# Optimization experiments

Measured on AMD Instinct MI355X. Metric: run time of the kernel, lower is better.

The kernel has to match this reference:

```python
import jax, jax.numpy as jnp
import numpy as np

B, N, D, H, F = 16, 257, 1024, 16, 4096
HD = D // H
EPS = 1e-5
GATING_TEMP = 0.25  # gating_hyperparam for steep_sigmoid
SCALE = HD ** -0.5


def layer_norm(x, g, b):
    mu = jnp.mean(x, axis=-1, keepdims=True)
    var = jnp.mean(jnp.square(x - mu), axis=-1, keepdims=True)
    return (x - mu) * jax.lax.rsqrt(var + EPS) * g + b


def quick_gelu(x):
    return x * jax.nn.sigmoid(1.702 * x)


def setup_inputs() -> dict:
    key = jax.random.key(0)
    ks = jax.random.split(key, 24)
    s = 0.02
    inp = {
        'hidden_states': jax.random.normal(ks[0], (B, N, D), jnp.float32),
        'cached_hidden': jax.random.normal(ks[1], (B, N, D), jnp.float32),
        'cached_q': jax.random.normal(ks[2], (B, N, D), jnp.float32),
        'cached_k': jax.random.normal(ks[3], (B, N, D), jnp.float32),
        'cached_v': jax.random.normal(ks[4], (B, N, D), jnp.float32),
        'ln1_g': jnp.ones((D,), jnp.float32),
        'ln1_b': jnp.zeros((D,), jnp.float32),
        'wq': jax.random.normal(ks[5], (D, D), jnp.float32) * s,
        'bq': jnp.zeros((D,), jnp.float32),
        'wk': jax.random.normal(ks[6], (D, D), jnp.float32) * s,
        'bk': jnp.zeros((D,), jnp.float32),
        'wv': jax.random.normal(ks[7], (D, D), jnp.float32) * s,
        'bv': jnp.zeros((D,), jnp.float32),
        'wo': jax.random.normal(ks[8], (D, D), jnp.float32) * s,
        'bo': jnp.zeros((D,), jnp.float32),
        'ln2_g': jnp.ones((D,), jnp.float32),
        'ln2_b': jnp.zeros((D,), jnp.float32),
        'w1': jax.random.normal(ks[9], (D, F), jnp.float32) * s,
        'b1': jnp.zeros((F,), jnp.float32),
        'w2': jax.random.normal(ks[10], (F, D), jnp.float32) * s,
        'b2': jnp.zeros((D,), jnp.float32),
        'threshold': jnp.float32(0.5),
    }
    return inp


def reference(hidden_states, cached_hidden, cached_q, cached_k, cached_v,
              ln1_g, ln1_b, wq, bq, wk, bk, wv, bv, wo, bo,
              ln2_g, ln2_b, w1, b1, w2, b2, threshold):
    # layer_norm1 + QKV projection (layer_norm1_qkv_projection)
    h_ln = layer_norm(hidden_states, ln1_g, ln1_b)
    q = h_ln @ wq + bq
    k = h_ln @ wk + bk
    v = h_ln @ wv + bv

    # reuse module: cosine^1 similarity vs cached hidden, steep_sigmoid gating
    # against learned threshold; soft gather/scatter blend of cached states.
    num = jnp.sum(cached_hidden * hidden_states, axis=-1)           # [B,N]
    den = (jnp.linalg.norm(cached_hidden, axis=-1)
           * jnp.linalg.norm(hidden_states, axis=-1) + 1e-8)
    sim = num / den                                                 # [B,N]
    gate = jax.nn.sigmoid((sim - threshold) / GATING_TEMP)[..., None]  # [B,N,1]

    hidden = gate * cached_hidden + (1.0 - gate) * hidden_states
    q = gate * cached_q + (1.0 - gate) * q
    k = gate * cached_k + (1.0 - gate) * k
    v = gate * cached_v + (1.0 - gate) * v

    # manual bmm-softmax-bmm attention
    qh = (q * SCALE).reshape(B, N, H, HD).transpose(0, 2, 1, 3)  # [B,H,N,hd]
    kh = k.reshape(B, N, H, HD).transpose(0, 2, 1, 3)
    vh = v.reshape(B, N, H, HD).transpose(0, 2, 1, 3)
    scores = jnp.einsum('bhqd,bhkd->bhqk', qh, kh)
    probs = jax.nn.softmax(scores, axis=-1)
    attn = jnp.einsum('bhqk,bhkd->bhqd', probs, vh)
    attn = attn.transpose(0, 2, 1, 3).reshape(B, N, D)
    attn = attn @ wo + bo

    hidden = hidden + attn
    residual = hidden
    hidden = layer_norm(hidden, ln2_g, ln2_b)
    hidden = quick_gelu(hidden @ w1 + b1) @ w2 + b2
    return residual + hidden
```

## Files before the change

### kernel.cpp

```cpp
#include <hip/hip_runtime.h>
#include <hip/hip_bf16.h>
#include <stdint.h>

#define BB   16
#define SEQ  257
#define DD   1024
#define NH   16
#define HD_  64
#define FF   4096
#define MM   (BB*SEQ)
#define MPAD 4224
#define SPAD 272
#define VPAD 288
#define SCALE_Q 0.125f

typedef __bf16 bf16x8 __attribute__((ext_vector_type(8)));
typedef float  f32x4  __attribute__((ext_vector_type(4)));
typedef unsigned short u16;

__device__ __forceinline__ u16 f2bf(float f) {
  uint32_t u = __float_as_uint(f);
  uint32_t r = (u + 0x7FFFu + ((u >> 16) & 1u)) >> 16;
  return (u16)r;
}
__device__ __forceinline__ float bf2f(u16 u) {
  return __uint_as_float(((uint32_t)u) << 16);
}
__device__ __forceinline__ void gll16(const void* g, void* l) {
  __builtin_amdgcn_global_load_lds(
      (const __attribute__((address_space(1))) void*)g,
      (__attribute__((address_space(3))) void*)l, 16, 0, 0);
}
__device__ __forceinline__ float wsum(float v) {
  #pragma unroll
  for (int o = 1; o < 64; o <<= 1) v += __shfl_xor(v, o);
  return v;
}

__global__ __launch_bounds__(256) void transpose_kernel(
    const float* __restrict__ in, u16* __restrict__ out, int R, int C) {
  __shared__ float tile[64][65];
  int ctiles = C >> 6;
  int r0 = (blockIdx.x / ctiles) << 6, c0 = (blockIdx.x % ctiles) << 6;
  int tx = threadIdx.x & 63, ty = threadIdx.x >> 6;
  #pragma unroll
  for (int it = 0; it < 16; ++it) {
    int rr = it * 4 + ty;
    tile[rr][tx] = in[(size_t)(r0 + rr) * C + c0 + tx];
  }
  __syncthreads();
  #pragma unroll
  for (int it = 0; it < 16; ++it) {
    int rr = it * 4 + ty;
    out[(size_t)(c0 + rr) * R + r0 + tx] = f2bf(tile[tx][rr]);
  }
}

__global__ __launch_bounds__(256) void ln1_gate_kernel(
    const float* __restrict__ h, const float* __restrict__ c,
    const float* __restrict__ g, const float* __restrict__ bta,
    const float* __restrict__ thr, u16* __restrict__ hln,
    float* __restrict__ hblend, float* __restrict__ gate) {
  int m = blockIdx.x, t = threadIdx.x, l = t & 63, w = t >> 6;
  const float4 hv = *(const float4*)(h + (size_t)m * DD + t * 4);
  const float4 cv = *(const float4*)(c + (size_t)m * DD + t * 4);
  float sh = hv.x + hv.y + hv.z + hv.w;
  float sh2 = hv.x*hv.x + hv.y*hv.y + hv.z*hv.z + hv.w*hv.w;
  float sch = hv.x*cv.x + hv.y*cv.y + hv.z*cv.z + hv.w*cv.w;
  float sc2 = cv.x*cv.x + cv.y*cv.y + cv.z*cv.z + cv.w*cv.w;
  sh = wsum(sh); sh2 = wsum(sh2); sch = wsum(sch); sc2 = wsum(sc2);
  __shared__ float red[4][4];
  if (l == 0) { red[w][0]=sh; red[w][1]=sh2; red[w][2]=sch; red[w][3]=sc2; }
  __syncthreads();
  float Sh  = red[0][0]+red[1][0]+red[2][0]+red[3][0];
  float Sh2 = red[0][1]+red[1][1]+red[2][1]+red[3][1];
  float Sch = red[0][2]+red[1][2]+red[2][2]+red[3][2];
  float Sc2 = red[0][3]+red[1][3]+red[2][3]+red[3][3];
  float mean = Sh * (1.f/DD);
  float var  = Sh2 * (1.f/DD) - mean*mean;
  float rs   = rsqrtf(var + 1e-5f);
  float sim  = Sch / (sqrtf(Sc2)*sqrtf(Sh2) + 1e-8f);
  float gv   = 1.f / (1.f + __expf(-(sim - thr[0]) * 4.0f));
  float4 gg = *(const float4*)(g + t*4);
  float4 bb = *(const float4*)(bta + t*4);
  ushort4 ob;
  ob.x = f2bf((hv.x-mean)*rs*gg.x + bb.x);
  ob.y = f2bf((hv.y-mean)*rs*gg.y + bb.y);
  ob.z = f2bf((hv.z-mean)*rs*gg.z + bb.z);
  ob.w = f2bf((hv.w-mean)*rs*gg.w + bb.w);
  *(ushort4*)(hln + (size_t)m * DD + t * 4) = ob;
  float4 hb;
  hb.x = gv*cv.x + (1.f-gv)*hv.x;  hb.y = gv*cv.y + (1.f-gv)*hv.y;
  hb.z = gv*cv.z + (1.f-gv)*hv.z;  hb.w = gv*cv.w + (1.f-gv)*hv.w;
  *(float4*)(hblend + (size_t)m * DD + t * 4) = hb;
  if (t == 0) gate[m] = gv;
}

__global__ __launch_bounds__(256) void ln2_kernel(
    const float* __restrict__ in, const float* __restrict__ g,
    const float* __restrict__ bta, u16* __restrict__ outb) {
  int m = blockIdx.x, t = threadIdx.x, l = t & 63, w = t >> 6;
  const float4 hv = *(const float4*)(in + (size_t)m * DD + t * 4);
  float sh = hv.x + hv.y + hv.z + hv.w;
  float sh2 = hv.x*hv.x + hv.y*hv.y + hv.z*hv.z + hv.w*hv.w;
  sh = wsum(sh); sh2 = wsum(sh2);
  __shared__ float red[4][2];
  if (l == 0) { red[w][0] = sh; red[w][1] = sh2; }
  __syncthreads();
  float Sh  = red[0][0]+red[1][0]+red[2][0]+red[3][0];
  float Sh2 = red[0][1]+red[1][1]+red[2][1]+red[3][1];
  float mean = Sh * (1.f/DD);
  float rs = rsqrtf(Sh2 * (1.f/DD) - mean*mean + 1e-5f);
  float4 gg = *(const float4*)(g + t*4);
  float4 bb = *(const float4*)(bta + t*4);
  ushort4 ob;
  ob.x = f2bf((hv.x-mean)*rs*gg.x + bb.x);
  ob.y = f2bf((hv.y-mean)*rs*gg.y + bb.y);
  ob.z = f2bf((hv.z-mean)*rs*gg.z + bb.z);
  ob.w = f2bf((hv.w-mean)*rs*gg.w + bb.w);
  *(ushort4*)(outb + (size_t)m * DD + t * 4) = ob;
}

template<int EPI>
__global__ __launch_bounds__(256) void gemm_bt(
    const u16* __restrict__ A, const u16* __restrict__ Bt, int K,
    const float* __restrict__ bias,
    const float* __restrict__ gate,
    const float* __restrict__ c0, const float* __restrict__ c1, const float* __restrict__ c2,
    const float* __restrict__ bq, const float* __restrict__ bk, const float* __restrict__ bv,
    u16* __restrict__ qb, u16* __restrict__ kb, u16* __restrict__ vt,
    const float* __restrict__ addsrc, float* __restrict__ outf, u16* __restrict__ outb) {
  const int tid = threadIdx.x, w = tid >> 6, l = tid & 63, lr = l & 15, lh = l >> 4;
  const int n0 = blockIdx.x * 128, m0 = blockIdx.y * 128;
  const int wm = w >> 1, wn = w & 1;
  __shared__ u16 sA[128 * 32], sB[128 * 32];
  f32x4 acc[4][4];
  f32x4 zero = {0.f, 0.f, 0.f, 0.f};
  #pragma unroll
  for (int i = 0; i < 4; ++i)
    #pragma unroll
    for (int j = 0; j < 4; ++j) acc[i][j] = zero;

  const int r0 = tid >> 2, cc = (tid & 3) * 8;
  const u16* ga0 = A  + (size_t)(m0 + r0) * K + cc;
  const u16* ga1 = A  + (size_t)(m0 + 64 + r0) * K + cc;
  const u16* gb0 = Bt + (size_t)(n0 + r0) * K + cc;
  const u16* gb1 = Bt + (size_t)(n0 + 64 + r0) * K + cc;
  u16* lA0 = &sA[w * 512];  u16* lA1 = &sA[2048 + w * 512];
  u16* lB0 = &sB[w * 512];  u16* lB1 = &sB[2048 + w * 512];

  for (int k0 = 0; k0 < K; k0 += 32) {
    __syncthreads();
    gll16(ga0 + k0, lA0);  gll16(ga1 + k0, lA1);
    gll16(gb0 + k0, lB0);  gll16(gb1 + k0, lB1);
    __syncthreads();
    bf16x8 af[4], bfr[4];
    #pragma unroll
    for (int mi = 0; mi < 4; ++mi)
      af[mi] = *(const bf16x8*)&sA[(wm*64 + mi*16 + lr)*32 + lh*8];
    #pragma unroll
    for (int ni = 0; ni < 4; ++ni)
      bfr[ni] = *(const bf16x8*)&sB[(wn*64 + ni*16 + lr)*32 + lh*8];
    #pragma unroll
    for (int mi = 0; mi < 4; ++mi)
      #pragma unroll
      for (int ni = 0; ni < 4; ++ni)
        acc[mi][ni] = __builtin_amdgcn_mfma_f32_16x16x32_bf16(af[mi], bfr[ni], acc[mi][ni], 0, 0, 0);
  }

  if constexpr (EPI == 0) {
    const int which = n0 >> 10;
    const float* cb = which==0 ? bq : (which==1 ? bk : bv);
    const float* cp = which==0 ? c0 : (which==1 ? c1 : c2);
    const float scl = which==0 ? SCALE_Q : 1.0f;
    #pragma unroll
    for (int mi = 0; mi < 4; ++mi) {
      #pragma unroll
      for (int r = 0; r < 4; ++r) {
        const int row = m0 + wm*64 + mi*16 + lh*4 + r;
        if (row < MM) {
          const float gv = gate[row];
          const int bidx = row / SEQ, nn = row - bidx * SEQ;
          #pragma unroll
          for (int ni = 0; ni < 4; ++ni) {
            const int col = n0 + wn*64 + ni*16 + lr;
            const int d = col & 1023, hd = d & 63, hh = d >> 6;
            const float lin = acc[mi][ni][r] + cb[d];
            const float val = (gv * cp[(size_t)row*DD + d] + (1.f - gv) * lin) * scl;
            if (which == 2)
              vt[((size_t)(bidx*NH + hh)*HD_ + hd)*VPAD + nn] = f2bf(val);
            else {
              u16* dst = which==0 ? qb : kb;
              dst[((size_t)(bidx*NH + hh)*SPAD + nn)*HD_ + hd] = f2bf(val);
            }
          }
        }
      }
    }
  } else if constexpr (EPI == 1) {
    #pragma unroll
    for (int mi = 0; mi < 4; ++mi)
      #pragma unroll
      for (int r = 0; r < 4; ++r) {
        const int row = m0 + wm*64 + mi*16 + lh*4 + r;
        if (row < MM) {
          #pragma unroll
          for (int ni = 0; ni < 4; ++ni) {
            const int col = n0 + wn*64 + ni*16 + lr;
            outf[(size_t)row*DD + col] = acc[mi][ni][r] + bias[col] + addsrc[(size_t)row*DD + col];
          }
        }
      }
  } else {
    #pragma unroll
    for (int mi = 0; mi < 4; ++mi)
      #pragma unroll
      for (int r = 0; r < 4; ++r) {
        const int row = m0 + wm*64 + mi*16 + lh*4 + r;
        if (row < MM) {
          #pragma unroll
          for (int ni = 0; ni < 4; ++ni) {
            const int col = n0 + wn*64 + ni*16 + lr;
            const float x = acc[mi][ni][r] + bias[col];
            const float s = 1.f / (1.f + __expf(-1.702f * x));
            outb[(size_t)row*FF + col] = f2bf(x * s);
          }
        }
      }
  }
}

__global__ __launch_bounds__(256) void attn_kernel(
    const u16* __restrict__ qb, const u16* __restrict__ kb,
    const u16* __restrict__ vt, u16* __restrict__ attn_out) {
  __shared__ u16 P[64 * 296];
  const int bh = blockIdx.x, b = bh >> 4, hh = bh & 15;
  const int q0 = blockIdx.y * 64;
  const int tid = threadIdx.x, w = tid >> 6, l = tid & 63, lr = l & 15, lh = l >> 4;
  const u16* qp = qb + (size_t)bh * SPAD * HD_;
  const u16* kp = kb + (size_t)bh * SPAD * HD_;
  const u16* vp = vt + (size_t)bh * HD_ * VPAD;

  const int qr = q0 + w*16 + lr;
  const int qrc = qr < 271 ? qr : 271;
  bf16x8 aq0 = *(const bf16x8*)(qp + (size_t)qrc*HD_ + lh*8);
  bf16x8 aq1 = *(const bf16x8*)(qp + (size_t)qrc*HD_ + 32 + lh*8);

  f32x4 st[18];
  f32x4 zero = {0.f,0.f,0.f,0.f};
  #pragma unroll
  for (int t = 0; t < 18; ++t) st[t] = zero;
  #pragma unroll
  for (int t = 0; t < 18; ++t) {
    int key = t*16 + lr;  int keyc = key < 271 ? key : 271;
    bf16x8 b0 = *(const bf16x8*)(kp + (size_t)keyc*HD_ + lh*8);
    bf16x8 b1 = *(const bf16x8*)(kp + (size_t)keyc*HD_ + 32 + lh*8);
    st[t] = __builtin_amdgcn_mfma_f32_16x16x32_bf16(aq0, b0, st[t], 0, 0, 0);
    st[t] = __builtin_amdgcn_mfma_f32_16x16x32_bf16(aq1, b1, st[t], 0, 0, 0);
  }
  #pragma unroll
  for (int t = 0; t < 18; ++t) {
    int key = t*16 + lr;
    if (key >= SEQ) { st[t][0]=-1e30f; st[t][1]=-1e30f; st[t][2]=-1e30f; st[t][3]=-1e30f; }
  }
  float mr[4], sr[4];
  #pragma unroll
  for (int r = 0; r < 4; ++r) {
    float m = st[0][r];
    #pragma unroll
    for (int t = 1; t < 18; ++t) m = fmaxf(m, st[t][r]);
    m = fmaxf(m, __shfl_xor(m, 1));  m = fmaxf(m, __shfl_xor(m, 2));
    m = fmaxf(m, __shfl_xor(m, 4));  m = fmaxf(m, __shfl_xor(m, 8));
    mr[r] = m;  sr[r] = 0.f;
  }
  #pragma unroll
  for (int t = 0; t < 18; ++t)
    #pragma unroll
    for (int r = 0; r < 4; ++r) {
      float p = __expf(st[t][r] - mr[r]);
      st[t][r] = p;  sr[r] += p;
    }
  #pragma unroll
  for (int r = 0; r < 4; ++r) {
    sr[r] += __shfl_xor(sr[r], 1);  sr[r] += __shfl_xor(sr[r], 2);
    sr[r] += __shfl_xor(sr[r], 4);  sr[r] += __shfl_xor(sr[r], 8);
  }
  #pragma unroll
  for (int t = 0; t < 18; ++t)
    #pragma unroll
    for (int r = 0; r < 4; ++r)
      P[(w*16 + lh*4 + r)*296 + t*16 + lr] = f2bf(st[t][r]);
  __syncthreads();

  f32x4 o[4];
  #pragma unroll
  for (int ni = 0; ni < 4; ++ni) o[ni] = zero;
  #pragma unroll
  for (int ks = 0; ks < 9; ++ks) {
    bf16x8 pa = *(const bf16x8*)&P[(w*16 + lr)*296 + ks*32 + lh*8];
    #pragma unroll
    for (int ni = 0; ni < 4; ++ni) {
      bf16x8 bv_ = *(const bf16x8*)(vp + (size_t)(ni*16 + lr)*VPAD + ks*32 + lh*8);
      o[ni] = __builtin_amdgcn_mfma_f32_16x16x32_bf16(pa, bv_, o[ni], 0, 0, 0);
    }
  }
  #pragma unroll
  for (int r = 0; r < 4; ++r) {
    const int qrow = q0 + w*16 + lh*4 + r;
    if (qrow < SEQ) {
      const float inv = 1.f / sr[r];
      #pragma unroll
      for (int ni = 0; ni < 4; ++ni)
        attn_out[(size_t)(b*SEQ + qrow)*DD + hh*HD_ + ni*16 + lr] = f2bf(o[ni][r] * inv);
    }
  }
}

extern "C" void kernel_launch(void* const* d_in, const int* in_sizes, int n_in,
                              void* d_out, int out_size, void* d_ws, size_t ws_size,
                              hipStream_t stream) {
  (void)in_sizes; (void)n_in; (void)out_size; (void)ws_size;
  const float* hidden   = (const float*)d_in[0];
  const float* cached_h = (const float*)d_in[1];
  const float* cached_q = (const float*)d_in[2];
  const float* cached_k = (const float*)d_in[3];
  const float* cached_v = (const float*)d_in[4];
  const float* ln1_g = (const float*)d_in[5];
  const float* ln1_b = (const float*)d_in[6];
  const float* wq = (const float*)d_in[7];
  const float* bq = (const float*)d_in[8];
  const float* wk = (const float*)d_in[9];
  const float* bk = (const float*)d_in[10];
  const float* wv = (const float*)d_in[11];
  const float* bv = (const float*)d_in[12];
  const float* wo = (const float*)d_in[13];
  const float* bo = (const float*)d_in[14];
  const float* ln2_g = (const float*)d_in[15];
  const float* ln2_b = (const float*)d_in[16];
  const float* w1 = (const float*)d_in[17];
  const float* b1 = (const float*)d_in[18];
  const float* w2 = (const float*)d_in[19];
  const float* b2 = (const float*)d_in[20];
  const float* thr = (const float*)d_in[21];
  float* out = (float*)d_out;

  char* ws = (char*)d_ws;
  size_t off = 0;
  auto alloc = [&](size_t bytes) {
    void* p = ws + off;  off += (bytes + 255) & ~(size_t)255;  return p;
  };
  u16*   wqkvT  = (u16*)alloc(3072ull * 1024 * 2);
  u16*   woT    = (u16*)alloc(1024ull * 1024 * 2);
  u16*   w1T    = (u16*)alloc(4096ull * 1024 * 2);
  u16*   w2T    = (u16*)alloc(1024ull * 4096 * 2);
  float* gate   = (float*)alloc((size_t)MPAD * 4);
  float* resid2 = (float*)alloc((size_t)MPAD * DD * 4);
  u16*   regA   = (u16*)alloc((size_t)MPAD * DD * 2);
  u16 *hln = regA, *attn_o = regA, *ln2out = regA;
  char*  regB   = (char*)alloc(44200448ull);
  u16*   qbuf   = (u16*)regB;
  u16*   kbuf   = (u16*)(regB + 8912896ull);
  u16*   vtb    = (u16*)(regB + 2ull*8912896);
  float* hblend = (float*)(regB + 2ull*8912896 + 9437184ull);
  u16*   mid    = (u16*)regB;

  dim3 blk(256);
  transpose_kernel<<<dim3(256),  blk, 0, stream>>>(wq, wqkvT,                 1024, 1024);
  transpose_kernel<<<dim3(256),  blk, 0, stream>>>(wk, wqkvT + 1024*1024,     1024, 1024);
  transpose_kernel<<<dim3(256),  blk, 0, stream>>>(wv, wqkvT + 2*1024*1024,   1024, 1024);
  transpose_kernel<<<dim3(256),  blk, 0, stream>>>(wo, woT,                   1024, 1024);
  transpose_kernel<<<dim3(1024), blk, 0, stream>>>(w1, w1T,                   1024, 4096);
  transpose_kernel<<<dim3(1024), blk, 0, stream>>>(w2, w2T,                   4096, 1024);

  ln1_gate_kernel<<<dim3(MM), blk, 0, stream>>>(hidden, cached_h, ln1_g, ln1_b, thr,
                                                hln, hblend, gate);

  gemm_bt<0><<<dim3(24, 33), blk, 0, stream>>>(hln, wqkvT, 1024, nullptr,
      gate, cached_q, cached_k, cached_v, bq, bk, bv, qbuf, kbuf, vtb,
      nullptr, nullptr, nullptr);

  attn_kernel<<<dim3(256, 5), blk, 0, stream>>>(qbuf, kbuf, vtb, attn_o);

  gemm_bt<1><<<dim3(8, 33), blk, 0, stream>>>(attn_o, woT, 1024, bo,
      nullptr, nullptr, nullptr, nullptr, nullptr, nullptr, nullptr,
      nullptr, nullptr, nullptr, hblend, resid2, nullptr);

  ln2_kernel<<<dim3(MM), blk, 0, stream>>>(resid2, ln2_g, ln2_b, ln2out);

  gemm_bt<2><<<dim3(32, 33), blk, 0, stream>>>(ln2out, w1T, 1024, b1,
      nullptr, nullptr, nullptr, nullptr, nullptr, nullptr, nullptr,
      nullptr, nullptr, nullptr, nullptr, nullptr, mid);

  gemm_bt<1><<<dim3(8, 33), blk, 0, stream>>>(mid, w2T, 4096, b2,
      nullptr, nullptr, nullptr, nullptr, nullptr, nullptr, nullptr,
      nullptr, nullptr, nullptr, resid2, out, nullptr);
}
```

Measured before the change: 364.9 us.

## Double-buffer GEMM LDS tiles and move V transpose to a separate kernel

The bf16 GEMM main loop now uses two LDS buffers, issuing async global-to-LDS loads for the next K tile while computing on the current one, which removes one barrier per iteration. The QKV epilogue writes V in the same head-major row layout as Q and K instead of scattering into a transposed buffer. A new vtrans_kernel then transposes V through LDS with coalesced writes. This targets the uncoalesced strided stores in the V epilogue and the load latency in the main loop, at the cost of an extra kernel launch, an extra pass over V, and more LDS per block.

Result: faster. 332.7 us (-8.8%).

```diff
diff --git a/kernel.cpp b/kernel.cpp
--- a/kernel.cpp
+++ b/kernel.cpp
@@ -23,9 +23,6 @@
   uint32_t r = (u + 0x7FFFu + ((u >> 16) & 1u)) >> 16;
   return (u16)r;
 }
-__device__ __forceinline__ float bf2f(u16 u) {
-  return __uint_as_float(((uint32_t)u) << 16);
-}
 __device__ __forceinline__ void gll16(const void* g, void* l) {
   __builtin_amdgcn_global_load_lds(
       (const __attribute__((address_space(1))) void*)g,
@@ -53,6 +50,28 @@
   for (int it = 0; it < 16; ++it) {
     int rr = it * 4 + ty;
     out[(size_t)(c0 + rr) * R + r0 + tx] = f2bf(tile[tx][rr]);
+  }
+}
+
+__global__ __launch_bounds__(256) void vtrans_kernel(
+    const u16* __restrict__ vb, u16* __restrict__ vt) {
+  __shared__ u16 tile[64][72];
+  const int bh = blockIdx.x, c = blockIdx.y;
+  const int tx = threadIdx.x & 63, ty = threadIdx.x >> 6;
+  const u16* src = vb + (size_t)bh * SPAD * HD_;
+  u16* dst = vt + (size_t)bh * HD_ * VPAD;
+  #pragma unroll
+  for (int it = 0; it < 16; ++it) {
+    int r = it * 4 + ty;
+    int nn = c * 64 + r;  int nnc = nn < SPAD ? nn : SPAD - 1;
+    tile[r][tx] = src[(size_t)nnc * HD_ + tx];
+  }
+  __syncthreads();
+  #pragma unroll
+  for (int it = 0; it < 16; ++it) {
+    int hd = it * 4 + ty;
+    int col = c * 64 + tx;
+    if (col < VPAD) dst[(size_t)hd * VPAD + col] = tile[tx][hd];
   }
 }
 
@@ -128,12 +147,12 @@
     const float* __restrict__ gate,
     const float* __restrict__ c0, const float* __restrict__ c1, const float* __restrict__ c2,
     const float* __restrict__ bq, const float* __restrict__ bk, const float* __restrict__ bv,
-    u16* __restrict__ qb, u16* __restrict__ kb, u16* __restrict__ vt,
+    u16* __restrict__ qb, u16* __restrict__ kb, u16* __restrict__ vb,
     const float* __restrict__ addsrc, float* __restrict__ outf, u16* __restrict__ outb) {
   const int tid = threadIdx.x, w = tid >> 6, l = tid & 63, lr = l & 15, lh = l >> 4;
   const int n0 = blockIdx.x * 128, m0 = blockIdx.y * 128;
   const int wm = w >> 1, wn = w & 1;
-  __shared__ u16 sA[128 * 32], sB[128 * 32];
+  __shared__ u16 sA[2][4096], sB[2][4096];
   f32x4 acc[4][4];
   f32x4 zero = {0.f, 0.f, 0.f, 0.f};
   #pragma unroll
@@ -146,21 +165,26 @@
   const u16* ga1 = A  + (size_t)(m0 + 64 + r0) * K + cc;
   const u16* gb0 = Bt + (size_t)(n0 + r0) * K + cc;
   const u16* gb1 = Bt + (size_t)(n0 + 64 + r0) * K + cc;
-  u16* lA0 = &sA[w * 512];  u16* lA1 = &sA[2048 + w * 512];
-  u16* lB0 = &sB[w * 512];  u16* lB1 = &sB[2048 + w * 512];
-
-  for (int k0 = 0; k0 < K; k0 += 32) {
+
+  const int nt = K >> 5;
+  gll16(ga0, &sA[0][w*512]);  gll16(ga1, &sA[0][2048 + w*512]);
+  gll16(gb0, &sB[0][w*512]);  gll16(gb1, &sB[0][2048 + w*512]);
+
+  for (int t = 0; t < nt; ++t) {
+    const int cur = t & 1;
     __syncthreads();
-    gll16(ga0 + k0, lA0);  gll16(ga1 + k0, lA1);
-    gll16(gb0 + k0, lB0);  gll16(gb1 + k0, lB1);
-    __syncthreads();
+    if (t + 1 < nt) {
+      const int k0 = (t + 1) << 5;
+      gll16(ga0 + k0, &sA[cur^1][w*512]);  gll16(ga1 + k0, &sA[cur^1][2048 + w*512]);
+      gll16(gb0 + k0, &sB[cur^1][w*512]);  gll16(gb1 + k0, &sB[cur^1][2048 + w*512]);
+    }
     bf16x8 af[4], bfr[4];
     #pragma unroll
     for (int mi = 0; mi < 4; ++mi)
-      af[mi] = *(const bf16x8*)&sA[(wm*64 + mi*16 + lr)*32 + lh*8];
+      af[mi] = *(const bf16x8*)&sA[cur][(wm*64 + mi*16 + lr)*32 + lh*8];
     #pragma unroll
     for (int ni = 0; ni < 4; ++ni)
-      bfr[ni] = *(const bf16x8*)&sB[(wn*64 + ni*16 + lr)*32 + lh*8];
+      bfr[ni] = *(const bf16x8*)&sB[cur][(wn*64 + ni*16 + lr)*32 + lh*8];
     #pragma unroll
     for (int mi = 0; mi < 4; ++mi)
       #pragma unroll
@@ -172,6 +196,7 @@
     const int which = n0 >> 10;
     const float* cb = which==0 ? bq : (which==1 ? bk : bv);
     const float* cp = which==0 ? c0 : (which==1 ? c1 : c2);
+    u16* dst = which==0 ? qb : (which==1 ? kb : vb);
     const float scl = which==0 ? SCALE_Q : 1.0f;
     #pragma unroll
     for (int mi = 0; mi < 4; ++mi) {
@@ -187,12 +212,7 @@
             const int d = col & 1023, hd = d & 63, hh = d >> 6;
             const float lin = acc[mi][ni][r] + cb[d];
             const float val = (gv * cp[(size_t)row*DD + d] + (1.f - gv) * lin) * scl;
-            if (which == 2)
-              vt[((size_t)(bidx*NH + hh)*HD_ + hd)*VPAD + nn] = f2bf(val);
-            else {
-              u16* dst = which==0 ? qb : kb;
-              dst[((size_t)(bidx*NH + hh)*SPAD + nn)*HD_ + hd] = f2bf(val);
-            }
+            dst[((size_t)(bidx*NH + hh)*SPAD + nn)*HD_ + hd] = f2bf(val);
           }
         }
       }
@@ -357,11 +377,14 @@
   float* resid2 = (float*)alloc((size_t)MPAD * DD * 4);
   u16*   regA   = (u16*)alloc((size_t)MPAD * DD * 2);
   u16 *hln = regA, *attn_o = regA, *ln2out = regA;
-  char*  regB   = (char*)alloc(44200448ull);
+  const size_t QKV_B = (size_t)256 * SPAD * HD_ * 2;
+  const size_t VT_B  = (size_t)256 * HD_ * VPAD * 2;
+  char*  regB   = (char*)alloc(3*QKV_B + VT_B + (size_t)MPAD * DD * 4);
   u16*   qbuf   = (u16*)regB;
-  u16*   kbuf   = (u16*)(regB + 8912896ull);
-  u16*   vtb    = (u16*)(regB + 2ull*8912896);
-  float* hblend = (float*)(regB + 2ull*8912896 + 9437184ull);
+  u16*   kbuf   = (u16*)(regB + QKV_B);
+  u16*   vbuf   = (u16*)(regB + 2*QKV_B);
+  u16*   vtb    = (u16*)(regB + 3*QKV_B);
+  float* hblend = (float*)(regB + 3*QKV_B + VT_B);
   u16*   mid    = (u16*)regB;
 
   dim3 blk(256);
@@ -376,8 +399,10 @@
                                                 hln, hblend, gate);
 
   gemm_bt<0><<<dim3(24, 33), blk, 0, stream>>>(hln, wqkvT, 1024, nullptr,
-      gate, cached_q, cached_k, cached_v, bq, bk, bv, qbuf, kbuf, vtb,
+      gate, cached_q, cached_k, cached_v, bq, bk, bv, qbuf, kbuf, vbuf,
       nullptr, nullptr, nullptr);
+
+  vtrans_kernel<<<dim3(256, 5), blk, 0, stream>>>(vbuf, vtb);
 
   attn_kernel<<<dim3(256, 5), blk, 0, stream>>>(qbuf, kbuf, vtb, attn_o);
 
```
